# Kernel optimization log

Hardware: AMD Instinct MI355X
Metric: run time of the kernel (lower is better)

The kernel has to match this reference:

```python
import jax, jax.numpy as jnp
import numpy as np

N_KERNELS = 5
MUL_FACTOR = 2.0
# bandwidth_multipliers = mul_factor ** (arange(n_kernels) - n_kernels // 2)
BW_MULTIPLIERS = MUL_FACTOR ** (np.arange(N_KERNELS) - N_KERNELS // 2)  # [0.25,0.5,1,2,4]


def setup_inputs() -> dict:
    key = jax.random.key(0)
    kx, ky = jax.random.split(key)
    X = jax.random.normal(kx, (4096, 64), dtype=jnp.float32)
    Y = jax.random.normal(ky, (4096, 64), dtype=jnp.float32)
    return {"X": X, "Y": Y}


def _mmd(X, Y):
    Z = jnp.vstack([X, Y])                      # [N, d], N = n + m
    n_total = Z.shape[0]
    # squared pairwise L2 distances (cdist(Z,Z)**2)
    sq = jnp.sum(Z * Z, axis=1)                 # [N]
    L2 = sq[:, None] + sq[None, :] - 2.0 * (Z @ Z.T)  # [N, N]
    L2 = jnp.maximum(L2, 0.0)
    # median heuristic bandwidth (mean of off-diag distances); torch uses .data -> stop_gradient
    bandwidth = jax.lax.stop_gradient(jnp.sum(L2)) / (n_total ** 2 - n_total)
    mults = jnp.asarray(BW_MULTIPLIERS, dtype=L2.dtype)  # [K]
    # sum over bandwidths of exp(-L2 / (bandwidth * mult))
    K = jnp.sum(jnp.exp(-L2[None, :, :] / (bandwidth * mults)[:, None, None]), axis=0)  # [N, N]
    nX = X.shape[0]
    XX = jnp.mean(K[:nX, :nX])
    XY = jnp.mean(K[:nX, nX:])
    YY = jnp.mean(K[nX:, nX:])
    return XX - 2.0 * XY + YY


def reference(X, Y):
    return _mmd(X, Y)
```

## Files before the change

### kernel.cpp

```cpp
#include <hip/hip_runtime.h>


#define NX 4096
#define NT 8192
#define DD 64
#define NBLK 32
#define NTRI (NBLK * (NBLK + 1) / 2)

using f32x4 = __attribute__((ext_vector_type(4))) float;
using s8v   = __attribute__((ext_vector_type(8))) short;

__device__ __forceinline__ float fast_exp2(float x) {
#if __has_builtin(__builtin_amdgcn_exp2f)
    return __builtin_amdgcn_exp2f(x);
#else
    return exp2f(x);
#endif
}
__device__ __forceinline__ ushort f2bf(float f) {
    unsigned u = __float_as_uint(f);
    unsigned r = u + 0x7fffu + ((u >> 16) & 1u);
    return (ushort)(r >> 16);
}

__global__ __launch_bounds__(512)
void k_prep(const float* __restrict__ X, const float* __restrict__ Y,
            ushort* __restrict__ ZH, float* __restrict__ sq,
            float* __restrict__ colsum, double* __restrict__ sumsq)
{
    __shared__ float  colred[64];
    __shared__ double ssred[8];
    const int tid = threadIdx.x, bid = blockIdx.x;
    const int sub = tid & 15;
    if (tid < 64) colred[tid] = 0.f;
    __syncthreads();

    float ca0 = 0.f, ca1 = 0.f, ca2 = 0.f, ca3 = 0.f, ssq = 0.f;
#pragma unroll
    for (int k = 0; k < 4; ++k) {
        const int row = bid * 128 + k * 32 + (tid >> 4);
        const float4* zr = (const float4*)((row < NX) ? (X + (size_t)row * DD)
                                                      : (Y + (size_t)(row - NX) * DD));
        float4 v = zr[sub];
        ((ushort4*)(ZH + (size_t)row * DD))[sub] =
            make_ushort4(f2bf(v.x), f2bf(v.y), f2bf(v.z), f2bf(v.w));
        float d = fmaf(v.x, v.x, fmaf(v.y, v.y, fmaf(v.z, v.z, v.w * v.w)));
        ssq += d;
        float dr = d;
#pragma unroll
        for (int m = 1; m < 16; m <<= 1) dr += __shfl_xor(dr, m);
        if (sub == 0) sq[row] = dr;
        ca0 += v.x; ca1 += v.y; ca2 += v.z; ca3 += v.w;
    }

    ca0 += __shfl_xor(ca0, 16); ca0 += __shfl_xor(ca0, 32);
    ca1 += __shfl_xor(ca1, 16); ca1 += __shfl_xor(ca1, 32);
    ca2 += __shfl_xor(ca2, 16); ca2 += __shfl_xor(ca2, 32);
    ca3 += __shfl_xor(ca3, 16); ca3 += __shfl_xor(ca3, 32);
    if ((tid & 63) < 16) {
        atomicAdd(&colred[sub * 4 + 0], ca0);
        atomicAdd(&colred[sub * 4 + 1], ca1);
        atomicAdd(&colred[sub * 4 + 2], ca2);
        atomicAdd(&colred[sub * 4 + 3], ca3);
    }
#pragma unroll
    for (int off = 32; off; off >>= 1) ssq += __shfl_down(ssq, off);
    if ((tid & 63) == 0) ssred[tid >> 6] = (double)ssq;
    __syncthreads();
    if (tid == 0) {
        double s = 0.0;
#pragma unroll
        for (int w = 0; w < 8; ++w) s += ssred[w];
        atomicAdd(sumsq, s);
    }
    if (tid < 64) atomicAdd(&colsum[tid], colred[tid]);
}

__global__ void k_bw(const double* __restrict__ sumsq, const float* __restrict__ colsum,
                     float* __restrict__ cs)
{
    const int lane = threadIdx.x;
    double cv = (double)colsum[lane]; cv *= cv;
#pragma unroll
    for (int m = 1; m < 64; m <<= 1) cv += __shfl_xor(cv, m);
    if (lane == 0) {
        double sl2 = 2.0 * (double)NT * sumsq[0] - 2.0 * cv;
        double bw = sl2 / ((double)NT * (double)NT - (double)NT);
        double s4 = -0.36067376022224085 / bw;
        cs[0] = (float)s4;
        cs[1] = (float)(-2.0 * s4);
    }
}

struct BFrag { s8v h[2][2]; };

__global__ __launch_bounds__(512, 4)
void k_main(const ushort* __restrict__ ZH, const float* __restrict__ sq,
            const float* __restrict__ cs,
            double* __restrict__ accS, unsigned* __restrict__ cnt,
            float* __restrict__ out)
{
    __shared__ double sred[8];
    const int tid = threadIdx.x, lane = tid & 63, wid = tid >> 6;
    const int wr = wid >> 1, wc = wid & 1;
    const int l15 = lane & 15, lh = lane >> 4;

    int t = blockIdx.x, bi = 0;
    while (t >= NBLK - bi) { t -= NBLK - bi; ++bi; }
    const int bj = bi + t;

    const int rbase = bi * 256 + wr * 64;
    const int jbase = bj * 256;
    const float s4 = cs[0], c2q = cs[1];

    s8v ah[4][2];
    f32x4 psi[4];
#pragma unroll
    for (int rg = 0; rg < 4; ++rg) {
#pragma unroll
        for (int ks = 0; ks < 2; ++ks)
            ah[rg][ks] = *(const s8v*)(ZH + (size_t)(rbase + rg * 16 + l15) * DD + ks * 32 + lh * 8);
        psi[rg] = s4 * (*(const f32x4*)(sq + rbase + rg * 16 + lh * 4));
    }

    double dsum = 0.0;

    auto LOADB = [&](BFrag& b, int tt) {
        const int cb = jbase + tt * 64 + wc * 32;
#pragma unroll
        for (int cg = 0; cg < 2; ++cg)
#pragma unroll
            for (int ks = 0; ks < 2; ++ks)
                b.h[cg][ks] = *(const s8v*)(ZH + (size_t)(cb + cg * 16 + l15) * DD + ks * 32 + lh * 8);
    };

    auto STEP = [&](const BFrag& b, int tt) {
        const int cb = jbase + tt * 64 + wc * 32;
        f32x4 acc[4][2];
#pragma unroll
        for (int rg = 0; rg < 4; ++rg)
#pragma unroll
            for (int cg = 0; cg < 2; ++cg)
                acc[rg][cg] = (f32x4){0.f, 0.f, 0.f, 0.f};
#pragma unroll
        for (int ks = 0; ks < 2; ++ks)
#pragma unroll
            for (int rg = 0; rg < 4; ++rg)
#pragma unroll
                for (int cg = 0; cg < 2; ++cg)
                    acc[rg][cg] = __builtin_amdgcn_mfma_f32_16x16x32_bf16(
                        ah[rg][ks], b.h[cg][ks], acc[rg][cg], 0, 0, 0);
        const float sj0 = s4 * sq[cb + l15];
        const float sj1 = s4 * sq[cb + 16 + l15];
        float bsum = 0.f;
#pragma unroll
        for (int rg = 0; rg < 4; ++rg)
#pragma unroll
            for (int cg = 0; cg < 2; ++cg) {
                const float sj = cg ? sj1 : sj0;
#pragma unroll
                for (int q = 0; q < 4; ++q) {
                    float x = fmaf(c2q, acc[rg][cg][q], psi[rg][q] + sj);
                    x = fminf(x, 0.f);
                    float v  = fast_exp2(x);
                    float v2 = v * v, v4 = v2 * v2, v8 = v4 * v4, v16 = v8 * v8;
                    bsum += ((v16 + v8) + (v4 + v2)) + v;
                }
            }
        dsum += (double)bsum;
    };

    BFrag b0, b1;
    LOADB(b0, 0);
    LOADB(b1, 1);
    STEP(b0, 0);
    LOADB(b0, 2);
    STEP(b1, 1);
    LOADB(b1, 3);
    STEP(b0, 2);
    STEP(b1, 3);

#pragma unroll
    for (int off = 32; off; off >>= 1) dsum += __shfl_down(dsum, off);
    if (lane == 0) sred[wid] = dsum;
    __syncthreads();
    if (tid == 0) {
        double bsum = 0.0;
#pragma unroll
        for (int w = 0; w < 8; ++w) bsum += sred[w];
        const bool pos = (bi < 16) == (bj < 16);
        const double wt = (bi == bj) ? 1.0 : 2.0;
        atomicAdd(accS, pos ? wt * bsum : -wt * bsum);
        __threadfence();
        unsigned old = atomicAdd(cnt, 1u);
        if (old == (unsigned)NTRI - 1u) {
            double S = atomicAdd(accS, 0.0);
            out[0] = (float)(S * (1.0 / ((double)NX * (double)NX)));
        }
    }
}

extern "C" void kernel_launch(void* const* d_in, const int* in_sizes, int n_in,
                              void* d_out, int out_size, void* d_ws, size_t ws_size,
                              hipStream_t stream)
{
    const float* X = (const float*)d_in[0];
    const float* Y = (const float*)d_in[1];

    char* ws = (char*)d_ws;
    double*   sumsq  = (double*)(ws + 0);
    double*   accS   = (double*)(ws + 8);
    unsigned* cnt    = (unsigned*)(ws + 16);
    float*    cs     = (float*)(ws + 24);
    float*    colsum = (float*)(ws + 64);
    float*    sq     = (float*)(ws + 512);
    ushort*   ZH     = (ushort*)(ws + 65536);

    hipMemsetAsync(d_ws, 0, 512, stream);
    k_prep<<<64, 512, 0, stream>>>(X, Y, ZH, sq, colsum, sumsq);
    k_bw  <<<1, 64, 0, stream>>>(sumsq, colsum, cs);
    k_main<<<NTRI, 512, 0, stream>>>(ZH, sq, cs, accS, cnt, (float*)d_out);
}
```

Before: 92.98 us.

## Use smaller triangular tiles, fold bandwidth kernel into prep, and bin the atomics

The main kernel now uses 128x128 tiles with 256-thread blocks over a 64x64 block triangle, so there are many more, smaller blocks to spread across the GPU. The triangle index is computed in closed form with a sqrt instead of a loop. The separate bandwidth kernel is removed: the last prep block, found with an atomic counter, computes the scale factors, which saves one launch. The single global double atomic is split into 32 padded bins to reduce contention, and the final block sums the bins. Per-column squared norms are hoisted out of the inner step.

```diff
diff --git a/kernel.cpp b/kernel.cpp
--- a/kernel.cpp
+++ b/kernel.cpp
@@ -4,8 +4,10 @@
 #define NX 4096
 #define NT 8192
 #define DD 64
-#define NBLK 32
+#define NBLK 64
 #define NTRI (NBLK * (NBLK + 1) / 2)
+#define NBIN 32
+#define BINSTRIDE 8
 
 using f32x4 = __attribute__((ext_vector_type(4))) float;
 using s8v   = __attribute__((ext_vector_type(8))) short;
@@ -26,7 +28,8 @@
 __global__ __launch_bounds__(512)
 void k_prep(const float* __restrict__ X, const float* __restrict__ Y,
             ushort* __restrict__ ZH, float* __restrict__ sq,
-            float* __restrict__ colsum, double* __restrict__ sumsq)
+            float* __restrict__ colsum, double* __restrict__ sumsq,
+            unsigned* __restrict__ prepcnt, float* __restrict__ cs)
 {
     __shared__ float  colred[64];
     __shared__ double ssred[8];
@@ -74,59 +77,64 @@
         atomicAdd(sumsq, s);
     }
     if (tid < 64) atomicAdd(&colsum[tid], colred[tid]);
-}
-
-__global__ void k_bw(const double* __restrict__ sumsq, const float* __restrict__ colsum,
-                     float* __restrict__ cs)
-{
-    const int lane = threadIdx.x;
-    double cv = (double)colsum[lane]; cv *= cv;
-#pragma unroll
-    for (int m = 1; m < 64; m <<= 1) cv += __shfl_xor(cv, m);
-    if (lane == 0) {
-        double sl2 = 2.0 * (double)NT * sumsq[0] - 2.0 * cv;
-        double bw = sl2 / ((double)NT * (double)NT - (double)NT);
-        double s4 = -0.36067376022224085 / bw;
-        cs[0] = (float)s4;
-        cs[1] = (float)(-2.0 * s4);
+
+    __threadfence();
+    __syncthreads();
+    if (tid == 0) {
+        if (atomicAdd(prepcnt, 1u) == 63u) {
+            double s2 = 0.0;
+            for (int c = 0; c < 64; ++c) { double v = (double)colsum[c]; s2 += v * v; }
+            double sl2 = 2.0 * (double)NT * sumsq[0] - 2.0 * s2;
+            double bw  = sl2 / ((double)NT * (double)NT - (double)NT);
+            double s4  = -0.36067376022224085 / bw;
+            cs[0] = (float)s4;
+            cs[1] = (float)(-2.0 * s4);
+        }
     }
 }
 
 struct BFrag { s8v h[2][2]; };
 
-__global__ __launch_bounds__(512, 4)
+__global__ __launch_bounds__(256, 5)
 void k_main(const ushort* __restrict__ ZH, const float* __restrict__ sq,
             const float* __restrict__ cs,
-            double* __restrict__ accS, unsigned* __restrict__ cnt,
+            double* __restrict__ accbin, unsigned* __restrict__ cnt,
             float* __restrict__ out)
 {
-    __shared__ double sred[8];
+    __shared__ double sred[4];
     const int tid = threadIdx.x, lane = tid & 63, wid = tid >> 6;
-    const int wr = wid >> 1, wc = wid & 1;
     const int l15 = lane & 15, lh = lane >> 4;
 
-    int t = blockIdx.x, bi = 0;
-    while (t >= NBLK - bi) { t -= NBLK - bi; ++bi; }
-    const int bj = bi + t;
-
-    const int rbase = bi * 256 + wr * 64;
-    const int jbase = bj * 256;
+    const int t = blockIdx.x;
+    int bi = (int)((129.0 - __builtin_sqrt(16641.0 - 8.0 * (double)t)) * 0.5);
+    while (bi * (129 - bi) / 2 > t) --bi;
+    while ((bi + 1) * (129 - (bi + 1)) / 2 <= t) ++bi;
+    const int bj = bi + (t - bi * (129 - bi) / 2);
+
+    const int rbase = bi * 128 + wid * 32;
+    const int jbase = bj * 128;
     const float s4 = cs[0], c2q = cs[1];
 
-    s8v ah[4][2];
-    f32x4 psi[4];
-#pragma unroll
-    for (int rg = 0; rg < 4; ++rg) {
+    s8v ah[2][2];
+    f32x4 psi[2];
+#pragma unroll
+    for (int rg = 0; rg < 2; ++rg) {
 #pragma unroll
         for (int ks = 0; ks < 2; ++ks)
             ah[rg][ks] = *(const s8v*)(ZH + (size_t)(rbase + rg * 16 + l15) * DD + ks * 32 + lh * 8);
         psi[rg] = s4 * (*(const f32x4*)(sq + rbase + rg * 16 + lh * 4));
     }
+    float sjv[4][2];
+#pragma unroll
+    for (int tt = 0; tt < 4; ++tt) {
+        sjv[tt][0] = s4 * sq[jbase + tt * 32 + l15];
+        sjv[tt][1] = s4 * sq[jbase + tt * 32 + 16 + l15];
+    }
 
     double dsum = 0.0;
 
     auto LOADB = [&](BFrag& b, int tt) {
-        const int cb = jbase + tt * 64 + wc * 32;
+        const int cb = jbase + tt * 32;
 #pragma unroll
         for (int cg = 0; cg < 2; ++cg)
 #pragma unroll
@@ -135,29 +143,26 @@
     };
 
     auto STEP = [&](const BFrag& b, int tt) {
-        const int cb = jbase + tt * 64 + wc * 32;
-        f32x4 acc[4][2];
-#pragma unroll
-        for (int rg = 0; rg < 4; ++rg)
+        f32x4 acc[2][2];
+#pragma unroll
+        for (int rg = 0; rg < 2; ++rg)
 #pragma unroll
             for (int cg = 0; cg < 2; ++cg)
                 acc[rg][cg] = (f32x4){0.f, 0.f, 0.f, 0.f};
 #pragma unroll
         for (int ks = 0; ks < 2; ++ks)
 #pragma unroll
-            for (int rg = 0; rg < 4; ++rg)
+            for (int rg = 0; rg < 2; ++rg)
 #pragma unroll
                 for (int cg = 0; cg < 2; ++cg)
                     acc[rg][cg] = __builtin_amdgcn_mfma_f32_16x16x32_bf16(
                         ah[rg][ks], b.h[cg][ks], acc[rg][cg], 0, 0, 0);
-        const float sj0 = s4 * sq[cb + l15];
-        const float sj1 = s4 * sq[cb + 16 + l15];
         float bsum = 0.f;
 #pragma unroll
-        for (int rg = 0; rg < 4; ++rg)
+        for (int rg = 0; rg < 2; ++rg)
 #pragma unroll
             for (int cg = 0; cg < 2; ++cg) {
-                const float sj = cg ? sj1 : sj0;
+                const float sj = sjv[tt][cg];
 #pragma unroll
                 for (int q = 0; q < 4; ++q) {
                     float x = fmaf(c2q, acc[rg][cg][q], psi[rg][q] + sj);
@@ -185,16 +190,16 @@
     if (lane == 0) sred[wid] = dsum;
     __syncthreads();
     if (tid == 0) {
-        double bsum = 0.0;
-#pragma unroll
-        for (int w = 0; w < 8; ++w) bsum += sred[w];
-        const bool pos = (bi < 16) == (bj < 16);
+        double bsum = sred[0] + sred[1] + sred[2] + sred[3];
+        const bool pos = (bi < 32) == (bj < 32);
         const double wt = (bi == bj) ? 1.0 : 2.0;
-        atomicAdd(accS, pos ? wt * bsum : -wt * bsum);
+        atomicAdd(&accbin[(blockIdx.x & (NBIN - 1)) * BINSTRIDE],
+                  pos ? wt * bsum : -wt * bsum);
         __threadfence();
         unsigned old = atomicAdd(cnt, 1u);
         if (old == (unsigned)NTRI - 1u) {
-            double S = atomicAdd(accS, 0.0);
+            double S = 0.0;
+            for (int bq = 0; bq < NBIN; ++bq) S += accbin[bq * BINSTRIDE];
             out[0] = (float)(S * (1.0 / ((double)NX * (double)NX)));
         }
     }
@@ -208,16 +213,16 @@
     const float* Y = (const float*)d_in[1];
 
     char* ws = (char*)d_ws;
-    double*   sumsq  = (double*)(ws + 0);
-    double*   accS   = (double*)(ws + 8);
-    unsigned* cnt    = (unsigned*)(ws + 16);
-    float*    cs     = (float*)(ws + 24);
-    float*    colsum = (float*)(ws + 64);
-    float*    sq     = (float*)(ws + 512);
-    ushort*   ZH     = (ushort*)(ws + 65536);
-
-    hipMemsetAsync(d_ws, 0, 512, stream);
-    k_prep<<<64, 512, 0, stream>>>(X, Y, ZH, sq, colsum, sumsq);
-    k_bw  <<<1, 64, 0, stream>>>(sumsq, colsum, cs);
-    k_main<<<NTRI, 512, 0, stream>>>(ZH, sq, cs, accS, cnt, (float*)d_out);
-}
+    double*   sumsq   = (double*)(ws + 0);
+    unsigned* cnt     = (unsigned*)(ws + 16);
+    unsigned* prepcnt = (unsigned*)(ws + 20);
+    float*    cs      = (float*)(ws + 24);
+    float*    colsum  = (float*)(ws + 64);
+    double*   accbin  = (double*)(ws + 512);
+    float*    sq      = (float*)(ws + 4096);
+    ushort*   ZH      = (ushort*)(ws + 65536);
+
+    hipMemsetAsync(d_ws, 0, 4096, stream);
+    k_prep<<<64, 512, 0, stream>>>(X, Y, ZH, sq, colsum, sumsq, prepcnt, cs);
+    k_main<<<NTRI, 256, 0, stream>>>(ZH, sq, cs, accbin, cnt, (float*)d_out);
+}
```

Measured after the change: 114.9 us. +23.6%, slower.
